# Kernel tuning notes

Measured on AMD Instinct MI355X. Metric: run time of the kernel, lower is better.

Reference implementation:

```python
import jax, jax.numpy as jnp
import numpy as np
import math

B, L, D, H = 4, 2048, 1024, 16
HD = D // H


def setup_inputs() -> dict:
    key = jax.random.key(0)
    k1, k2, k3 = jax.random.split(key, 3)
    x = jax.random.normal(k1, (B, L, D), dtype=jnp.float32)
    # Linear weights stored as [in, out] so y = x @ W (equivalent to torch x @ W.T)
    Wqkv = jax.random.normal(k2, (D, 3 * D), dtype=jnp.float32) * (1.0 / math.sqrt(D))
    Wproj = jax.random.normal(k3, (D, D), dtype=jnp.float32) * (1.0 / math.sqrt(D))
    attn_mask = jnp.tril(jnp.ones((L, L), dtype=bool))  # True = attend (causal)
    key_padding_mask = jnp.zeros((B, L), dtype=bool)     # True = padded (none here)
    return {"x": x, "Wqkv": Wqkv, "Wproj": Wproj,
            "attn_mask": attn_mask, "key_padding_mask": key_padding_mask}


def reference(x, Wqkv, Wproj, attn_mask, key_padding_mask):
    Bx, Lx, Dx = x.shape
    qkv = x @ Wqkv                              # [B, L, 3D]
    q, k, v = jnp.split(qkv, 3, axis=-1)
    def shape(t):
        return t.reshape(Bx, Lx, H, HD).transpose(0, 2, 1, 3)  # [B, H, L, hd]
    q, k, v = shape(q), shape(k), shape(v)
    att = jnp.einsum('bhqd,bhkd->bhqk', q, k) / math.sqrt(HD)  # [B, H, L, L]
    neg_inf = jnp.float32(-jnp.inf)
    att = jnp.where(attn_mask[None, None, :, :], att, neg_inf)
    att = jnp.where(key_padding_mask[:, None, None, :], neg_inf, att)
    att = jax.nn.softmax(att, axis=-1)
    y = jnp.einsum('bhqk,bhkd->bhqd', att, v)   # [B, H, L, hd]
    y = y.transpose(0, 2, 1, 3).reshape(Bx, Lx, Dx)
    return y @ Wproj
```

## Files before the change

kernel.cpp:

```cpp
#include <hip/hip_runtime.h>
#include <cstdint>
#include <cstddef>


typedef __attribute__((ext_vector_type(8))) __bf16 bf16x8;
typedef __attribute__((ext_vector_type(4))) __bf16 bf16x4;
typedef __attribute__((ext_vector_type(4))) float f32x4;

__device__ __forceinline__ f32x4 mfma_bf16(bf16x8 a, bf16x8 b, f32x4 c) {
  return __builtin_amdgcn_mfma_f32_16x16x32_bf16(a, b, c, 0, 0, 0);
}

__device__ __forceinline__ void async_copy16(const void* gsrc, void* ldsdst) {
  __builtin_amdgcn_global_load_lds(
      (const __attribute__((address_space(1))) void*)gsrc,
      (__attribute__((address_space(3))) void*)ldsdst, 16, 0, 0);
}

__global__ __launch_bounds__(256) void f32_to_bf16(
    const float* __restrict__ in, __bf16* __restrict__ out) {
  const size_t i = ((size_t)blockIdx.x * 256 + threadIdx.x) * 4;
  const float4 v = *(const float4*)&in[i];
  bf16x4 o = {(__bf16)v.x, (__bf16)v.y, (__bf16)v.z, (__bf16)v.w};
  *(bf16x4*)&out[i] = o;
}

__global__ __launch_bounds__(256) void transpose_f32_bf16(
    const float* __restrict__ in, __bf16* __restrict__ out, int R, int C) {
  __shared__ float tile[32][33];
  const int c0 = blockIdx.x * 32;
  const int r0 = blockIdx.y * 32;
  const int tx = threadIdx.x & 31;
  const int ty = threadIdx.x >> 5;
#pragma unroll
  for (int i = 0; i < 32; i += 8)
    tile[ty + i][tx] = in[(size_t)(r0 + ty + i) * C + c0 + tx];
  __syncthreads();
#pragma unroll
  for (int i = 0; i < 32; i += 8)
    out[(size_t)(c0 + ty + i) * R + r0 + tx] = (__bf16)tile[tx][ty + i];
}


__global__ __launch_bounds__(256) void gemm_bt_f32out(
    const __bf16* __restrict__ A, const __bf16* __restrict__ BT,
    float* __restrict__ C, int M, int N, int K) {
  __shared__ __bf16 As[128 * 32];
  __shared__ __bf16 Bs[128 * 32];
  const int tid = threadIdx.x;
  const int wave = tid >> 6;
  const int lane = tid & 63;
  const int n16 = lane & 15;
  const int quad = lane >> 4;
  const int m0 = blockIdx.x * 128;
  const int n0 = blockIdx.y * 128;
  const int wr = wave >> 1;
  const int wc = wave & 1;

  const f32x4 zero = {0.f, 0.f, 0.f, 0.f};
  f32x4 acc[4][4];
#pragma unroll
  for (int i = 0; i < 4; ++i)
#pragma unroll
    for (int j = 0; j < 4; ++j) acc[i][j] = zero;

  const int KT = K >> 5;
  for (int kt = 0; kt < KT; ++kt) {
    const int k0 = kt << 5;
#pragma unroll
    for (int r = 0; r < 2; ++r) {
      const int li = (r << 8) + tid;
      const int row = li >> 2;
      const int kp8 = (li & 3) << 3;
      const int lbase = ((r << 8) + (wave << 6)) << 3;
      async_copy16(&A[(size_t)(m0 + row) * K + k0 + kp8], &As[lbase]);
      async_copy16(&BT[(size_t)(n0 + row) * K + k0 + kp8], &Bs[lbase]);
    }
    __syncthreads();
    bf16x8 af[4], bf[4];
#pragma unroll
    for (int t = 0; t < 4; ++t) {
      af[t] = *(const bf16x8*)&As[(wr * 64 + t * 16 + n16) * 32 + quad * 8];
      bf[t] = *(const bf16x8*)&Bs[(wc * 64 + t * 16 + n16) * 32 + quad * 8];
    }
#pragma unroll
    for (int mt = 0; mt < 4; ++mt)
#pragma unroll
      for (int nt = 0; nt < 4; ++nt)
        acc[mt][nt] = mfma_bf16(af[mt], bf[nt], acc[mt][nt]);
    __syncthreads();
  }
#pragma unroll
  for (int mt = 0; mt < 4; ++mt) {
#pragma unroll
    for (int r = 0; r < 4; ++r) {
      const int m = m0 + wr * 64 + mt * 16 + quad * 4 + r;
#pragma unroll
      for (int nt = 0; nt < 4; ++nt) {
        const int n = n0 + wc * 64 + nt * 16 + n16;
        C[(size_t)m * N + n] = acc[mt][nt][r];
      }
    }
  }
}

__global__ __launch_bounds__(256) void gemm_qkv(
    const __bf16* __restrict__ A, const __bf16* __restrict__ BT,
    __bf16* __restrict__ Q, __bf16* __restrict__ Kh, __bf16* __restrict__ VT) {
  __shared__ __bf16 As[128 * 32];
  __shared__ __bf16 Bs[128 * 32];
  const int tid = threadIdx.x;
  const int wave = tid >> 6;
  const int lane = tid & 63;
  const int n16 = lane & 15;
  const int quad = lane >> 4;
  const int m0 = blockIdx.x * 128;
  const int n0 = blockIdx.y * 128;
  const int wr = wave >> 1;
  const int wc = wave & 1;
  const int K = 1024;

  const f32x4 zero = {0.f, 0.f, 0.f, 0.f};
  f32x4 acc[4][4];
#pragma unroll
  for (int i = 0; i < 4; ++i)
#pragma unroll
    for (int j = 0; j < 4; ++j) acc[i][j] = zero;

  for (int kt = 0; kt < 32; ++kt) {
    const int k0 = kt << 5;
#pragma unroll
    for (int r = 0; r < 2; ++r) {
      const int li = (r << 8) + tid;
      const int row = li >> 2;
      const int kp8 = (li & 3) << 3;
      const int lbase = ((r << 8) + (wave << 6)) << 3;
      async_copy16(&A[(size_t)(m0 + row) * K + k0 + kp8], &As[lbase]);
      async_copy16(&BT[(size_t)(n0 + row) * K + k0 + kp8], &Bs[lbase]);
    }
    __syncthreads();
    bf16x8 af[4], bf[4];
#pragma unroll
    for (int t = 0; t < 4; ++t) {
      af[t] = *(const bf16x8*)&As[(wr * 64 + t * 16 + n16) * 32 + quad * 8];
      bf[t] = *(const bf16x8*)&Bs[(wc * 64 + t * 16 + n16) * 32 + quad * 8];
    }
#pragma unroll
    for (int mt = 0; mt < 4; ++mt)
#pragma unroll
      for (int nt = 0; nt < 4; ++nt)
        acc[mt][nt] = mfma_bf16(af[mt], bf[nt], acc[mt][nt]);
    __syncthreads();
  }

  const int b = m0 >> 11;
  if (n0 < 2048) {
    const float QSCALE = 0.125f * 1.44269504089f;
    const bool isQ = (n0 < 1024);
#pragma unroll
    for (int mt = 0; mt < 4; ++mt) {
#pragma unroll
      for (int r = 0; r < 4; ++r) {
        const int m = m0 + wr * 64 + mt * 16 + quad * 4 + r;
        const int l = m & 2047;
#pragma unroll
        for (int nt = 0; nt < 4; ++nt) {
          const int n = n0 + wc * 64 + nt * 16 + n16;
          const int d = n & 1023;
          const size_t bh = (size_t)(b * 16 + (d >> 6));
          const size_t idx = (bh * 2048 + l) * 64 + (d & 63);
          if (isQ)
            Q[idx] = (__bf16)(acc[mt][nt][r] * QSCALE);
          else
            Kh[idx] = (__bf16)acc[mt][nt][r];
        }
      }
    }
  } else {
    __syncthreads();
    __bf16* tw = (wave < 2 ? As : Bs) + (wave & 1) * 2048;
    const int h = ((n0 - 2048) >> 6) + wc;
    const size_t bhead = (size_t)(b * 16 + h);
    const int l0w = (m0 & 2047) + wr * 64;
#pragma unroll
    for (int pass = 0; pass < 2; ++pass) {
#pragma unroll
      for (int nt = 2 * pass; nt < 2 * pass + 2; ++nt) {
#pragma unroll
        for (int mt = 0; mt < 4; ++mt)
#pragma unroll
          for (int r = 0; r < 4; ++r) {
            const int hdp = (nt & 1) * 16 + n16;
            const int mm = mt * 16 + quad * 4 + r;
            const int chunk = mm >> 3;
            const int phys = chunk ^ (hdp & 7);
            tw[hdp * 64 + phys * 8 + (mm & 7)] = (__bf16)acc[mt][nt][r];
          }
      }
#pragma unroll
      for (int i = 0; i < 4; ++i) {
        const int c = lane + 64 * i;
        const int row = c >> 3;
        const int phys = (c & 7) ^ (row & 7);
        const bf16x8 v = *(const bf16x8*)&tw[row * 64 + phys * 8];
        *(bf16x8*)&VT[(bhead * 64 + pass * 32 + row) * 2048 + l0w +
                      (c & 7) * 8] = v;
      }
    }
  }
}

__global__ __launch_bounds__(256, 4) void flash_attn(
    const __bf16* __restrict__ Q, const __bf16* __restrict__ Kh,
    const __bf16* __restrict__ VT, __bf16* __restrict__ Y) {
  __shared__ __bf16 KsB[2][32 * 64];
  __shared__ __bf16 VsB[2][64 * 32];
  __shared__ __bf16 Ps[4][16 * 40];
  const int bh = blockIdx.x;
  const int p = blockIdx.y;
  const int tid = threadIdx.x;
  const int wave = tid >> 6;
  const int lane = tid & 63;
  const int n16 = lane & 15;
  const int quad = lane >> 4;
  __bf16* pb = Ps[wave];
  const __bf16* Qb = Q + (size_t)bh * 2048 * 64;
  const __bf16* Kb = Kh + (size_t)bh * 2048 * 64;
  const __bf16* Vb = VT + (size_t)bh * 64 * 2048;
  const int b = bh >> 4;
  const int h = bh & 15;
  const f32x4 zero = {0.f, 0.f, 0.f, 0.f};

  const int krow = wave * 8 + (lane >> 3);
  const int kcol8 = (((lane & 7) ^ (lane >> 3)) << 3);
  const int vrow = wave * 16 + (lane >> 2);
  const int vcol8 = (((lane & 3) ^ quad) << 3);

#pragma unroll
  for (int t = 0; t < 2; ++t) {
    const int qt = t == 0 ? p : 31 - p;
    const int q0w = qt * 64 + wave * 16;

    bf16x8 qf[2];
#pragma unroll
    for (int kh = 0; kh < 2; ++kh)
      qf[kh] = *(const bf16x8*)&Qb[(size_t)(q0w + n16) * 64 + kh * 32 +
                                   quad * 8];

    f32x4 o[4];
#pragma unroll
    for (int j = 0; j < 4; ++j) o[j] = zero;
    float lsum[4] = {0.f, 0.f, 0.f, 0.f};

    const int nsteps = 2 * qt + 2;

    async_copy16(&Kb[(size_t)krow * 64 + kcol8], &KsB[0][wave * 512]);
    async_copy16(&Vb[(size_t)vrow * 2048 + vcol8], &VsB[0][wave * 512]);

    for (int kt = 0; kt < nsteps; ++kt) {
      const int buf = kt & 1;
      const int c0 = kt * 32;
      __syncthreads();
      if (kt + 1 < nsteps) {
        const int nb = buf ^ 1;
        const int cn = c0 + 32;
        async_copy16(&Kb[(size_t)(cn + krow) * 64 + kcol8],
                     &KsB[nb][wave * 512]);
        async_copy16(&Vb[(size_t)vrow * 2048 + cn + vcol8],
                     &VsB[nb][wave * 512]);
      }
      const __bf16* ks = KsB[buf];
      const __bf16* vs = VsB[buf];

      f32x4 s[2];
      s[0] = zero;
      s[1] = zero;
#pragma unroll
      for (int ct = 0; ct < 2; ++ct) {
#pragma unroll
        for (int kh = 0; kh < 2; ++kh) {
          const bf16x8 kf = *(const bf16x8*)&ks[(ct * 16 + n16) * 64 +
                                                (((kh * 4 + quad) ^ (n16 & 7))
                                                 << 3)];
          s[ct] = mfma_bf16(qf[kh], kf, s[ct]);
        }
      }
      if (kt >= 2 * qt) {
#pragma unroll
        for (int r = 0; r < 4; ++r) {
          const int rowq = q0w + quad * 4 + r;
#pragma unroll
          for (int ct = 0; ct < 2; ++ct) {
            const int col = c0 + ct * 16 + n16;
            float e = __builtin_amdgcn_exp2f(s[ct][r]);
            e = (col <= rowq) ? e : 0.f;
            s[ct][r] = e;
            lsum[r] += e;
          }
        }
      } else {
#pragma unroll
        for (int r = 0; r < 4; ++r)
#pragma unroll
          for (int ct = 0; ct < 2; ++ct) {
            const float e = __builtin_amdgcn_exp2f(s[ct][r]);
            s[ct][r] = e;
            lsum[r] += e;
          }
      }
#pragma unroll
      for (int ct = 0; ct < 2; ++ct)
#pragma unroll
        for (int r = 0; r < 4; ++r)
          pb[(quad * 4 + r) * 40 + ct * 16 + n16] = (__bf16)s[ct][r];
      const bf16x8 pa = *(const bf16x8*)&pb[n16 * 40 + quad * 8];
#pragma unroll
      for (int ht = 0; ht < 4; ++ht) {
        const bf16x8 vf = *(const bf16x8*)&vs[(ht * 16 + n16) * 32 +
                                              ((quad ^ (n16 >> 2)) << 3)];
        o[ht] = mfma_bf16(pa, vf, o[ht]);
      }
    }

#pragma unroll
    for (int r = 0; r < 4; ++r) {
      float l = lsum[r];
#pragma unroll
      for (int off = 1; off < 16; off <<= 1) l += __shfl_xor(l, off, 16);
      const float inv = 1.0f / l;
      const int row = q0w + quad * 4 + r;
#pragma unroll
      for (int ht = 0; ht < 4; ++ht)
        Y[(size_t)(b * 2048 + row) * 1024 + h * 64 + ht * 16 + n16] =
            (__bf16)(o[ht][r] * inv);
    }
  }
}

extern "C" void kernel_launch(void* const* d_in, const int* in_sizes, int n_in,
                              void* d_out, int out_size, void* d_ws,
                              size_t ws_size, hipStream_t stream) {
  const float* x = (const float*)d_in[0];
  const float* Wqkv = (const float*)d_in[1];
  const float* Wproj = (const float*)d_in[2];
  float* out = (float*)d_out;

  char* ws = (char*)d_ws;
  __bf16* xb = (__bf16*)ws;     ws += (size_t)8192 * 1024 * 2;
  __bf16* WqkvT = (__bf16*)ws;  ws += (size_t)3072 * 1024 * 2;
  __bf16* WprojT = (__bf16*)ws; ws += (size_t)1024 * 1024 * 2;
  __bf16* Qs = (__bf16*)ws;     ws += (size_t)64 * 2048 * 64 * 2;
  __bf16* Ks = (__bf16*)ws;     ws += (size_t)64 * 2048 * 64 * 2;
  __bf16* VTs = (__bf16*)ws;    ws += (size_t)64 * 64 * 2048 * 2;
  __bf16* attn = xb;

  f32_to_bf16<<<8192, 256, 0, stream>>>(x, xb);
  transpose_f32_bf16<<<dim3(96, 32), 256, 0, stream>>>(Wqkv, WqkvT, 1024, 3072);
  transpose_f32_bf16<<<dim3(32, 32), 256, 0, stream>>>(Wproj, WprojT, 1024, 1024);
  gemm_qkv<<<dim3(64, 24), 256, 0, stream>>>(xb, WqkvT, Qs, Ks, VTs);
  flash_attn<<<dim3(64, 16), 256, 0, stream>>>(Qs, Ks, VTs, attn);
  gemm_bt_f32out<<<dim3(64, 8), 256, 0, stream>>>(attn, WprojT, out,
                                                  8192, 1024, 1024);
}
```

Before: 266.7 us.

## Stage Q/K epilogue through swizzled LDS and transpose attention score tiles

```diff
diff --git a/kernel.cpp b/kernel.cpp
--- a/kernel.cpp
+++ b/kernel.cpp
@@ -153,35 +153,46 @@
     __syncthreads();
   }
 
+  __syncthreads();
   const int b = m0 >> 11;
+  __bf16* tw = (wave < 2 ? As : Bs) + (wave & 1) * 2048;
+  const int l0w = (m0 & 2047) + wr * 64;
+
   if (n0 < 2048) {
     const float QSCALE = 0.125f * 1.44269504089f;
     const bool isQ = (n0 < 1024);
-#pragma unroll
-    for (int mt = 0; mt < 4; ++mt) {
-#pragma unroll
-      for (int r = 0; r < 4; ++r) {
-        const int m = m0 + wr * 64 + mt * 16 + quad * 4 + r;
-        const int l = m & 2047;
-#pragma unroll
-        for (int nt = 0; nt < 4; ++nt) {
-          const int n = n0 + wc * 64 + nt * 16 + n16;
-          const int d = n & 1023;
-          const size_t bh = (size_t)(b * 16 + (d >> 6));
-          const size_t idx = (bh * 2048 + l) * 64 + (d & 63);
-          if (isQ)
-            Q[idx] = (__bf16)(acc[mt][nt][r] * QSCALE);
-          else
-            Kh[idx] = (__bf16)acc[mt][nt][r];
-        }
+    const int h = ((n0 & 1023) >> 6) + wc;
+    __bf16* dst = isQ ? Q : Kh;
+    const size_t base = ((size_t)(b * 16 + h) * 2048) * 64;
+#pragma unroll
+    for (int pass = 0; pass < 2; ++pass) {
+#pragma unroll
+      for (int mt = 2 * pass; mt < 2 * pass + 2; ++mt) {
+#pragma unroll
+        for (int nt = 0; nt < 4; ++nt)
+#pragma unroll
+          for (int r = 0; r < 4; ++r) {
+            const int hd = nt * 16 + n16;
+            const int mm = (mt & 1) * 16 + quad * 4 + r;
+            const float v =
+                isQ ? acc[mt][nt][r] * QSCALE : acc[mt][nt][r];
+            tw[mm * 64 + (((hd >> 3) ^ (mm & 7)) << 3) + (hd & 7)] =
+                (__bf16)v;
+          }
+      }
+#pragma unroll
+      for (int i = 0; i < 4; ++i) {
+        const int c = lane + 64 * i;
+        const int row = c >> 3;
+        const int hd0 = (c & 7) << 3;
+        const int phys = (c & 7) ^ (row & 7);
+        const bf16x8 v = *(const bf16x8*)&tw[row * 64 + phys * 8];
+        *(bf16x8*)&dst[base + (size_t)(l0w + pass * 32 + row) * 64 + hd0] = v;
       }
     }
   } else {
-    __syncthreads();
-    __bf16* tw = (wave < 2 ? As : Bs) + (wave & 1) * 2048;
     const int h = ((n0 - 2048) >> 6) + wc;
     const size_t bhead = (size_t)(b * 16 + h);
-    const int l0w = (m0 & 2047) + wr * 64;
 #pragma unroll
     for (int pass = 0; pass < 2; ++pass) {
 #pragma unroll
@@ -192,8 +203,7 @@
           for (int r = 0; r < 4; ++r) {
             const int hdp = (nt & 1) * 16 + n16;
             const int mm = mt * 16 + quad * 4 + r;
-            const int chunk = mm >> 3;
-            const int phys = chunk ^ (hdp & 7);
+            const int phys = (mm >> 3) ^ (hdp & 7);
             tw[hdp * 64 + phys * 8 + (mm & 7)] = (__bf16)acc[mt][nt][r];
           }
       }
@@ -250,7 +260,7 @@
     f32x4 o[4];
 #pragma unroll
     for (int j = 0; j < 4; ++j) o[j] = zero;
-    float lsum[4] = {0.f, 0.f, 0.f, 0.f};
+    float lsum = 0.f;
 
     const int nsteps = 2 * qt + 2;
 
@@ -282,37 +292,37 @@
           const bf16x8 kf = *(const bf16x8*)&ks[(ct * 16 + n16) * 64 +
                                                 (((kh * 4 + quad) ^ (n16 & 7))
                                                  << 3)];
-          s[ct] = mfma_bf16(qf[kh], kf, s[ct]);
+          s[ct] = mfma_bf16(kf, qf[kh], s[ct]);
         }
       }
       if (kt >= 2 * qt) {
-#pragma unroll
-        for (int r = 0; r < 4; ++r) {
-          const int rowq = q0w + quad * 4 + r;
-#pragma unroll
-          for (int ct = 0; ct < 2; ++ct) {
-            const int col = c0 + ct * 16 + n16;
+        const int myq = q0w + n16;
+#pragma unroll
+        for (int ct = 0; ct < 2; ++ct)
+#pragma unroll
+          for (int r = 0; r < 4; ++r) {
+            const int kcol = c0 + ct * 16 + quad * 4 + r;
             float e = __builtin_amdgcn_exp2f(s[ct][r]);
-            e = (col <= rowq) ? e : 0.f;
+            e = (kcol <= myq) ? e : 0.f;
             s[ct][r] = e;
-            lsum[r] += e;
+            lsum += e;
           }
-        }
       } else {
 #pragma unroll
-        for (int r = 0; r < 4; ++r)
-#pragma unroll
-          for (int ct = 0; ct < 2; ++ct) {
+        for (int ct = 0; ct < 2; ++ct)
+#pragma unroll
+          for (int r = 0; r < 4; ++r) {
             const float e = __builtin_amdgcn_exp2f(s[ct][r]);
             s[ct][r] = e;
-            lsum[r] += e;
+            lsum += e;
           }
       }
 #pragma unroll
-      for (int ct = 0; ct < 2; ++ct)
-#pragma unroll
-        for (int r = 0; r < 4; ++r)
-          pb[(quad * 4 + r) * 40 + ct * 16 + n16] = (__bf16)s[ct][r];
+      for (int ct = 0; ct < 2; ++ct) {
+        const bf16x4 pk = {(__bf16)s[ct][0], (__bf16)s[ct][1],
+                           (__bf16)s[ct][2], (__bf16)s[ct][3]};
+        *(bf16x4*)&pb[n16 * 40 + ct * 16 + quad * 4] = pk;
+      }
       const bf16x8 pa = *(const bf16x8*)&pb[n16 * 40 + quad * 8];
 #pragma unroll
       for (int ht = 0; ht < 4; ++ht) {
@@ -322,17 +332,17 @@
       }
     }
 
+    lsum += __shfl_xor(lsum, 16);
+    lsum += __shfl_xor(lsum, 32);
+    const float inv = 1.0f / lsum;
 #pragma unroll
     for (int r = 0; r < 4; ++r) {
-      float l = lsum[r];
-#pragma unroll
-      for (int off = 1; off < 16; off <<= 1) l += __shfl_xor(l, off, 16);
-      const float inv = 1.0f / l;
+      const float invr = __shfl(inv, quad * 4 + r);
       const int row = q0w + quad * 4 + r;
 #pragma unroll
       for (int ht = 0; ht < 4; ++ht)
         Y[(size_t)(b * 2048 + row) * 1024 + h * 64 + ht * 16 + n16] =
-            (__bf16)(o[ht][r] * inv);
+            (__bf16)(o[ht][r] * invr);
     }
   }
 }
```

Result: faster. 255.0 us (-4.4%).
